# Optimization experiments

Measured on AMD Instinct MI355X. Metric: run time of the kernel, lower is better.

The kernel has to match this reference:

```python
import jax, jax.numpy as jnp
import numpy as np
from jax.scipy.special import logsumexp

B = 4096        # batch_size
D = 512         # feature dim
C = 128         # class_num
TEMP_F = 0.5
TEMP_L = 1.0
LAMBDA1 = 0.5
LAMBDA2 = 0.5
COS_EPS = 1e-8  # torch CosineSimilarity eps


def setup_inputs() -> dict:
    key = jax.random.key(0)
    k1, k2, k3, k4, k5 = jax.random.split(key, 5)
    return {
        "h1": jax.random.normal(k1, (B, D), dtype=jnp.float32),
        "h2": jax.random.normal(k2, (B, D), dtype=jnp.float32),
        "q1": jax.random.uniform(k3, (B, C), dtype=jnp.float32),
        "q2": jax.random.uniform(k4, (B, C), dtype=jnp.float32),
        "confidence": jax.random.uniform(k5, (B,), dtype=jnp.float32),
    }


def _ntxent_from_sim(sim, half):
    """NT-Xent per-row loss given full sim matrix [2*half, 2*half].

    Key identity: logits row r = [pos_r, negatives_r] where negatives exclude
    cols {r, partner(r)} and pos_r = sim[r, partner(r)]. Hence
    CE(logits, 0) = logsumexp over row excluding only the diagonal, minus pos.
    """
    N = 2 * half
    pos = jnp.concatenate([jnp.diagonal(sim, offset=half),
                           jnp.diagonal(sim, offset=-half)], axis=0)  # [N]
    eye = jnp.eye(N, dtype=bool)
    sim_masked = jnp.where(eye, -jnp.inf, sim)
    lse = logsumexp(sim_masked, axis=1)  # [N]
    return lse - pos  # per-row CE loss


def _forward_feature(h_i, h_j, confidence):
    b = h_i.shape[0]
    h = jnp.concatenate([h_i, h_j], axis=0)              # [2B, D]
    sim = jnp.matmul(h, h.T) / TEMP_F                     # [2B, 2B]
    loss = _ntxent_from_sim(sim, b)                       # [2B]
    loss = loss * jnp.tile(confidence, 2)                 # confidence.repeat(2)
    return loss.mean()


def _forward_label(q_i, q_j):
    c = q_i.shape[1]
    p_i = q_i.sum(0)
    p_i = p_i / p_i.sum()
    ne_i = jnp.log(jnp.float32(c)) + (p_i * jnp.log(p_i)).sum()
    p_j = q_j.sum(0)
    p_j = p_j / p_j.sum()
    ne_j = jnp.log(jnp.float32(c)) + (p_j * jnp.log(p_j)).sum()
    entropy = ne_i + ne_j

    q = jnp.concatenate([q_i.T, q_j.T], axis=0)           # [2C, B]
    norms = jnp.linalg.norm(q, axis=1)                    # [2C]
    denom = jnp.maximum(norms[:, None] * norms[None, :], COS_EPS)
    sim = (q @ q.T) / denom / TEMP_L                      # [2C, 2C]
    loss = _ntxent_from_sim(sim, c)                       # [2C]
    return loss.mean() + entropy


def reference(h1, h2, q1, q2, confidence):
    loss_feat = _forward_feature(h1, h2, confidence)
    loss_label = _forward_label(q1, q2)
    return LAMBDA1 * loss_feat + LAMBDA2 * loss_label
```

## Files before the change

### kernel.cpp

```cpp
#include <hip/hip_runtime.h>

typedef __attribute__((ext_vector_type(8))) short short8;
typedef __attribute__((ext_vector_type(4))) float f32x4;

#define NROW 8192
#define D_SZ 512

#define HB_OFF     0u
#define SPARTL_OFF 0u
#define SGRAM_OFF  2097152u
#define PSUMP_OFF  2359296u
#define FPART_OFF  2363392u
#define POS_OFF    8388608u
#define MPART_OFF  8421376u
#define SPARTF_OFF 8683520u

__device__ __forceinline__ unsigned short f32_to_bf16(float f) {
  unsigned int u = __float_as_uint(f);
  u = (u + 0x7FFFu + ((u >> 16) & 1u)) >> 16;
  return (unsigned short)u;
}

__global__ void convert_kernel(const float* __restrict__ h1, const float* __restrict__ h2,
                               unsigned short* __restrict__ hb) {
  int tid = blockIdx.x * 256 + threadIdx.x;
  float4 v = (tid < 524288) ? reinterpret_cast<const float4*>(h1)[tid]
                            : reinterpret_cast<const float4*>(h2)[tid - 524288];
  ushort4 o;
  o.x = f32_to_bf16(v.x); o.y = f32_to_bf16(v.y);
  o.z = f32_to_bf16(v.z); o.w = f32_to_bf16(v.w);
  reinterpret_cast<ushort4*>(hb)[tid] = o;
}

__global__ __launch_bounds__(256, 2) void feature_kernel(
    const short* __restrict__ hb, float* __restrict__ pos,
    float* __restrict__ mpart, float* __restrict__ spart) {
  __shared__ short lds_s[32 * 512];
  const int tid = threadIdx.x;
  const int w = tid >> 6;
  const int lane = tid & 63;
  const int lo16 = lane & 15;
  const int grp = lane >> 4;
  const int cz = blockIdx.x;
  const int bt = blockIdx.y;
  const int Rw = bt * 128 + w * 32;

  short8 A[2][16];
#pragma unroll
  for (int rt = 0; rt < 2; ++rt) {
    const short* ab = hb + (Rw + rt * 16 + lo16) * D_SZ + grp * 8;
#pragma unroll
    for (int kk = 0; kk < 16; ++kk)
      A[rt][kk] = *reinterpret_cast<const short8*>(ab + kk * 32);
  }
#pragma unroll
  for (int rt = 0; rt < 2; ++rt)
#pragma unroll
    for (int kk = 0; kk < 16; ++kk)
      asm volatile("" : "+v"(A[rt][kk]));

  float m0 = -INFINITY, m1 = -INFINITY, s0 = 0.f, s1 = 0.f;
  const int r0 = Rw + lo16;
  const int r1 = Rw + 16 + lo16;
  const int p0 = (r0 + 4096) & 8191;
  const int p1 = (r1 + 4096) & 8191;
  const int swz = (lo16 & 7) << 3;

#pragma unroll 1
  for (int g = 0; g < 32; ++g) {
    const int cg = cz * 1024 + g * 32;
    __syncthreads();
#pragma unroll
    for (int i = 0; i < 8; ++i) {
      int ch = i * 256 + tid;
      int col = ch >> 6, k8 = ch & 63;
      short8 v = *reinterpret_cast<const short8*>(hb + (cg + col) * D_SZ + k8 * 8);
      int dst = col * D_SZ + ((k8 * 8) ^ ((col & 7) << 3));
      *reinterpret_cast<short8*>(&lds_s[dst]) = v;
    }
    __syncthreads();

    f32x4 acc00 = {0,0,0,0}, acc01 = {0,0,0,0}, acc10 = {0,0,0,0}, acc11 = {0,0,0,0};
#pragma unroll
    for (int kk = 0; kk < 16; ++kk) {
      const int k = kk * 32 + grp * 8;
      short8 B0 = *reinterpret_cast<const short8*>(&lds_s[lo16 * D_SZ + (k ^ swz)]);
      short8 B1 = *reinterpret_cast<const short8*>(&lds_s[(16 + lo16) * D_SZ + (k ^ swz)]);
      acc00 = __builtin_amdgcn_mfma_f32_16x16x32_bf16(B0, A[0][kk], acc00, 0, 0, 0);
      acc01 = __builtin_amdgcn_mfma_f32_16x16x32_bf16(B0, A[1][kk], acc01, 0, 0, 0);
      acc10 = __builtin_amdgcn_mfma_f32_16x16x32_bf16(B1, A[0][kk], acc10, 0, 0, 0);
      acc11 = __builtin_amdgcn_mfma_f32_16x16x32_bf16(B1, A[1][kk], acc11, 0, 0, 0);
    }

    const int cbase = cg + grp * 4;
    {
      float v[8];
#pragma unroll
      for (int j = 0; j < 4; ++j) { v[j] = acc00[j] * 2.f; v[4 + j] = acc10[j] * 2.f; }
#pragma unroll
      for (int j = 0; j < 4; ++j) {
        int c0 = cbase + j, c1 = cbase + 16 + j;
        if (c0 == p0) pos[r0] = v[j];
        if (c1 == p0) pos[r0] = v[4 + j];
        if (c0 == r0) v[j] = -INFINITY;
        if (c1 == r0) v[4 + j] = -INFINITY;
      }
      float tm = v[0];
#pragma unroll
      for (int i = 1; i < 8; ++i) tm = fmaxf(tm, v[i]);
      tm = fmaxf(tm, __shfl_xor(tm, 16));
      tm = fmaxf(tm, __shfl_xor(tm, 32));
      float mn = fmaxf(m0, tm);
      float e = 0.f;
#pragma unroll
      for (int i = 0; i < 8; ++i) e += __expf(v[i] - mn);
      e += __shfl_xor(e, 16);
      e += __shfl_xor(e, 32);
      s0 = s0 * __expf(m0 - mn) + e;
      m0 = mn;
    }
    {
      float v[8];
#pragma unroll
      for (int j = 0; j < 4; ++j) { v[j] = acc01[j] * 2.f; v[4 + j] = acc11[j] * 2.f; }
#pragma unroll
      for (int j = 0; j < 4; ++j) {
        int c0 = cbase + j, c1 = cbase + 16 + j;
        if (c0 == p1) pos[r1] = v[j];
        if (c1 == p1) pos[r1] = v[4 + j];
        if (c0 == r1) v[j] = -INFINITY;
        if (c1 == r1) v[4 + j] = -INFINITY;
      }
      float tm = v[0];
#pragma unroll
      for (int i = 1; i < 8; ++i) tm = fmaxf(tm, v[i]);
      tm = fmaxf(tm, __shfl_xor(tm, 16));
      tm = fmaxf(tm, __shfl_xor(tm, 32));
      float mn = fmaxf(m1, tm);
      float e = 0.f;
#pragma unroll
      for (int i = 0; i < 8; ++i) e += __expf(v[i] - mn);
      e += __shfl_xor(e, 16);
      e += __shfl_xor(e, 32);
      s1 = s1 * __expf(m1 - mn) + e;
      m1 = mn;
    }
  }

  if (grp == 0) {
    mpart[cz * NROW + r0] = m0; spart[cz * NROW + r0] = s0;
    mpart[cz * NROW + r1] = m1; spart[cz * NROW + r1] = s1;
  }
}

__global__ void combine_feature_kernel(const float* __restrict__ mpart,
                                       const float* __restrict__ spart,
                                       const float* __restrict__ pos,
                                       const float* __restrict__ conf,
                                       float* __restrict__ fpart) {
  __shared__ float red[256];
  int r = blockIdx.x * 256 + threadIdx.x;
  float M = -INFINITY;
#pragma unroll
  for (int k = 0; k < 8; ++k) M = fmaxf(M, mpart[k * NROW + r]);
  float S = 0.f;
#pragma unroll
  for (int k = 0; k < 8; ++k) S += spart[k * NROW + r] * __expf(mpart[k * NROW + r] - M);
  float lse = logf(S) + M;
  float loss = (lse - pos[r]) * conf[r & 4095];
  red[threadIdx.x] = loss;
  __syncthreads();
  for (int s = 128; s > 0; s >>= 1) {
    if (threadIdx.x < s) red[threadIdx.x] += red[threadIdx.x + s];
    __syncthreads();
  }
  if (threadIdx.x == 0) fpart[blockIdx.x] = red[0];
}

__global__ __launch_bounds__(256) void label_gemm_kernel(const float* __restrict__ q1,
                                                         const float* __restrict__ q2,
                                                         float* __restrict__ Spart) {
  __shared__ float As[32 * 64];
  __shared__ float Bs[32 * 32];
  const int t = threadIdx.x;
  const int kz = blockIdx.x >> 5;
  const int bi = (blockIdx.x & 31) >> 3;
  const int bj = blockIdx.x & 7;
  const int tx = t & 15, ty = t >> 4;
  float a[4][2];
#pragma unroll
  for (int dr = 0; dr < 4; ++dr)
#pragma unroll
    for (int dc = 0; dc < 2; ++dc) a[dr][dc] = 0.f;

  for (int ch = 0; ch < 16; ++ch) {
    const int kbase = kz * 512 + ch * 32;
    __syncthreads();
#pragma unroll
    for (int i = 0; i < 8; ++i) {
      int e = i * 256 + t;
      int kr = e >> 6, j = e & 63;
      int ca = bi * 64 + j;
      As[kr * 64 + j] = (ca < 128) ? q1[(kbase + kr) * 128 + ca]
                                   : q2[(kbase + kr) * 128 + ca - 128];
    }
#pragma unroll
    for (int i = 0; i < 4; ++i) {
      int e = i * 256 + t;
      int kr = e >> 5, j = e & 31;
      int cb = bj * 32 + j;
      Bs[kr * 32 + j] = (cb < 128) ? q1[(kbase + kr) * 128 + cb]
                                   : q2[(kbase + kr) * 128 + cb - 128];
    }
    __syncthreads();
#pragma unroll 8
    for (int k = 0; k < 32; ++k) {
      float4 Av = *reinterpret_cast<const float4*>(&As[k * 64 + ty * 4]);
      float2 Bv = *reinterpret_cast<const float2*>(&Bs[k * 32 + tx * 2]);
      a[0][0] += Av.x * Bv.x; a[0][1] += Av.x * Bv.y;
      a[1][0] += Av.y * Bv.x; a[1][1] += Av.y * Bv.y;
      a[2][0] += Av.z * Bv.x; a[2][1] += Av.z * Bv.y;
      a[3][0] += Av.w * Bv.x; a[3][1] += Av.w * Bv.y;
    }
  }
  float* outp = Spart + kz * 65536;
#pragma unroll
  for (int dr = 0; dr < 4; ++dr) {
    int r = bi * 64 + ty * 4 + dr;
    int c = bj * 32 + tx * 2;
    outp[r * 256 + c] = a[dr][0];
    outp[r * 256 + c + 1] = a[dr][1];
  }
}

__global__ void label_prep_kernel(const float* __restrict__ q1, const float* __restrict__ q2,
                                  const float* __restrict__ Spart, float* __restrict__ S,
                                  float* __restrict__ psum_part) {
  const int b = blockIdx.x, t = threadIdx.x;
  if (b < 256) {
    int e = b * 256 + t;
    float acc = 0.f;
#pragma unroll
    for (int kz = 0; kz < 8; ++kz) acc += Spart[kz * 65536 + e];
    S[e] = acc;
  } else {
    __shared__ float sd[256];
    int idx = b - 256;
    const float* q = (idx < 4) ? q1 : q2;
    int col = t & 127, half = t >> 7;
    int rbase = (idx & 3) * 1024 + half * 512;
    float acc = 0.f;
    for (int i = 0; i < 512; ++i) acc += q[(rbase + i) * 128 + col];
    sd[t] = acc;
    __syncthreads();
    if (t < 128) psum_part[idx * 128 + col] = sd[t] + sd[t + 128];
  }
}

__global__ __launch_bounds__(256) void label_final_kernel(
    const float* __restrict__ S, const float* __restrict__ psum_part,
    const float* __restrict__ fpart, float* __restrict__ out) {
  __shared__ float nrm[256], red[256], redl[256];
  __shared__ float entropy_sh, feat_sh;
  const int t = threadIdx.x;
  nrm[t] = sqrtf(fmaxf(S[t * 257], 0.f));
  const float* pp = psum_part + (t >> 7) * 512 + (t & 127);
  float v = pp[0] + pp[128] + pp[256] + pp[384];
  red[t] = v;
  redl[t] = v * logf(fmaxf(v, 1e-30f));
  __syncthreads();
  for (int s = 64; s > 0; s >>= 1) {
    if ((t & 127) < s) { red[t] += red[t + s]; redl[t] += redl[t + s]; }
    __syncthreads();
  }
  if (t == 0) {
    float tot1 = red[0], tot2 = red[128];
    float ne1 = logf(128.f) + (redl[0] / tot1 - logf(tot1));
    float ne2 = logf(128.f) + (redl[128] / tot2 - logf(tot2));
    entropy_sh = ne1 + ne2;
  }
  __syncthreads();
  red[t] = (t < 32) ? fpart[t] : 0.f;
  __syncthreads();
  for (int s = 128; s > 0; s >>= 1) {
    if (t < s) red[t] += red[t + s];
    __syncthreads();
  }
  if (t == 0) feat_sh = red[0];
  __syncthreads();

  const float nr = nrm[t];
  const float* Srow = S + t * 256;
  const int partner = (t + 128) & 255;
  float m = -INFINITY;
  for (int c = 0; c < 256; ++c) {
    if (c == t) continue;
    float sv = Srow[c] / fmaxf(nr * nrm[c], 1e-8f);
    m = fmaxf(m, sv);
  }
  float ssum = 0.f, posv = 0.f;
  for (int c = 0; c < 256; ++c) {
    float sv = Srow[c] / fmaxf(nr * nrm[c], 1e-8f);
    if (c == partner) posv = sv;
    if (c != t) ssum += __expf(sv - m);
  }
  float loss_r = (logf(ssum) + m) - posv;
  __syncthreads();
  red[t] = loss_r;
  __syncthreads();
  for (int s = 128; s > 0; s >>= 1) {
    if (t < s) red[t] += red[t + s];
    __syncthreads();
  }
  if (t == 0)
    out[0] = 0.5f * (feat_sh / 8192.f) + 0.5f * (red[0] / 256.f + entropy_sh);
}

extern "C" void kernel_launch(void* const* d_in, const int* in_sizes, int n_in,
                              void* d_out, int out_size, void* d_ws, size_t ws_size,
                              hipStream_t stream) {
  const float* h1 = (const float*)d_in[0];
  const float* h2 = (const float*)d_in[1];
  const float* q1 = (const float*)d_in[2];
  const float* q2 = (const float*)d_in[3];
  const float* conf = (const float*)d_in[4];
  float* out = (float*)d_out;
  char* ws = (char*)d_ws;

  unsigned short* hb = (unsigned short*)(ws + HB_OFF);
  float* pos    = (float*)(ws + POS_OFF);
  float* mpart  = (float*)(ws + MPART_OFF);
  float* spartf = (float*)(ws + SPARTF_OFF);
  float* SpartL = (float*)(ws + SPARTL_OFF);
  float* Sgram  = (float*)(ws + SGRAM_OFF);
  float* psump  = (float*)(ws + PSUMP_OFF);
  float* fpart  = (float*)(ws + FPART_OFF);

  convert_kernel<<<4096, 256, 0, stream>>>(h1, h2, hb);
  feature_kernel<<<dim3(8, 64), 256, 0, stream>>>((const short*)hb, pos, mpart, spartf);
  combine_feature_kernel<<<32, 256, 0, stream>>>(mpart, spartf, pos, conf, fpart);
  label_gemm_kernel<<<256, 256, 0, stream>>>(q1, q2, SpartL);
  label_prep_kernel<<<264, 256, 0, stream>>>(q1, q2, SpartL, Sgram, psump);
  label_final_kernel<<<1, 256, 0, stream>>>(Sgram, psump, fpart, out);
}
```

Measured before the change: 272.9 us.

## Retile feature GEMM into 256x256 LDS-staged blocks with async double buffering

The feature kernel is rewritten to use 512-thread blocks computing 256x256 output tiles. Both operands are staged through double-buffered LDS using global_load_lds, and the online logsumexp update runs once per 256-column tile instead of once per 32-column step. The label GEMM is retiled to 64x64 output tiles with a 16-way K split, and the prep and final kernels are adjusted to match. This is meant to raise MFMA reuse and overlap loads with compute, at the cost of a large register footprint (128 accumulator floats per thread) and more partial buffers.

```diff
diff --git a/kernel.cpp b/kernel.cpp
--- a/kernel.cpp
+++ b/kernel.cpp
@@ -8,12 +8,17 @@
 
 #define HB_OFF     0u
 #define SPARTL_OFF 0u
-#define SGRAM_OFF  2097152u
-#define PSUMP_OFF  2359296u
-#define FPART_OFF  2363392u
+#define SGRAM_OFF  4194304u
+#define PSUMP_OFF  4456448u
+#define FPART_OFF  4472832u
 #define POS_OFF    8388608u
 #define MPART_OFF  8421376u
 #define SPARTF_OFF 8683520u
+
+#define GLOAD_LDS(gp, lp)                                     \
+  __builtin_amdgcn_global_load_lds(                           \
+      (const __attribute__((address_space(1))) void*)(gp),    \
+      (__attribute__((address_space(3))) void*)(lp), 16, 0, 0)
 
 __device__ __forceinline__ unsigned short f32_to_bf16(float f) {
   unsigned int u = __float_as_uint(f);
@@ -32,125 +37,160 @@
   reinterpret_cast<ushort4*>(hb)[tid] = o;
 }
 
-__global__ __launch_bounds__(256, 2) void feature_kernel(
+__global__ __launch_bounds__(512, 2) void feature_kernel(
     const short* __restrict__ hb, float* __restrict__ pos,
     float* __restrict__ mpart, float* __restrict__ spart) {
-  __shared__ short lds_s[32 * 512];
+  __shared__ short lds_s[2][2][16384];
   const int tid = threadIdx.x;
   const int w = tid >> 6;
   const int lane = tid & 63;
   const int lo16 = lane & 15;
   const int grp = lane >> 4;
+  const int lo7 = lo16 & 7;
+  const int wr = w >> 2;
+  const int wc = w & 3;
   const int cz = blockIdx.x;
   const int bt = blockIdx.y;
-  const int Rw = bt * 128 + w * 32;
-
-  short8 A[2][16];
-#pragma unroll
-  for (int rt = 0; rt < 2; ++rt) {
-    const short* ab = hb + (Rw + rt * 16 + lo16) * D_SZ + grp * 8;
-#pragma unroll
-    for (int kk = 0; kk < 16; ++kk)
-      A[rt][kk] = *reinterpret_cast<const short8*>(ab + kk * 32);
-  }
-#pragma unroll
-  for (int rt = 0; rt < 2; ++rt)
-#pragma unroll
-    for (int kk = 0; kk < 16; ++kk)
-      asm volatile("" : "+v"(A[rt][kk]));
-
-  float m0 = -INFINITY, m1 = -INFINITY, s0 = 0.f, s1 = 0.f;
-  const int r0 = Rw + lo16;
-  const int r1 = Rw + 16 + lo16;
-  const int p0 = (r0 + 4096) & 8191;
-  const int p1 = (r1 + 4096) & 8191;
-  const int swz = (lo16 & 7) << 3;
+  const int R0 = bt * 256;
+  const int CZ0 = cz * 1024;
+
+  const int srow = tid >> 3;
+  const int csrc = (tid & 7) ^ (srow & 7);
+  const short* baseA = hb + (size_t)(R0 + srow) * D_SZ + csrc * 8;
+  const short* baseB = hb + (size_t)(CZ0 + srow) * D_SZ + csrc * 8;
+
+#define STAGE_STEP(ct_, bk_, buf_) do {                        \
+    const short* sa_ = baseA + (bk_) * 64;                     \
+    const short* sb_ = baseB + (ct_) * 131072 + (bk_) * 64;    \
+    short* da_ = &lds_s[buf_][0][tid * 8];                     \
+    short* db_ = &lds_s[buf_][1][tid * 8];                     \
+    GLOAD_LDS(sa_, da_);                  GLOAD_LDS(sb_, db_);                  \
+    GLOAD_LDS(sa_ + 32768, da_ + 4096);   GLOAD_LDS(sb_ + 32768, db_ + 4096);   \
+    GLOAD_LDS(sa_ + 65536, da_ + 8192);   GLOAD_LDS(sb_ + 65536, db_ + 8192);   \
+    GLOAD_LDS(sa_ + 98304, da_ + 12288);  GLOAD_LDS(sb_ + 98304, db_ + 12288);  \
+  } while (0)
+
+  float mrun[8], srun[8];
+#pragma unroll
+  for (int rf = 0; rf < 8; ++rf) { mrun[rf] = -INFINITY; srun[rf] = 0.f; }
+
+  f32x4 acc[4][8];
+#pragma unroll
+  for (int cf = 0; cf < 4; ++cf)
+#pragma unroll
+    for (int rf = 0; rf < 8; ++rf) acc[cf][rf] = (f32x4){0, 0, 0, 0};
+
+  const int rowbaseA = (wr * 128 + lo16) * 64;
+  const int colbaseB = (wc * 64 + lo16) * 64;
+
+  STAGE_STEP(0, 0, 0);
+  __syncthreads();
 
 #pragma unroll 1
-  for (int g = 0; g < 32; ++g) {
-    const int cg = cz * 1024 + g * 32;
-    __syncthreads();
-#pragma unroll
-    for (int i = 0; i < 8; ++i) {
-      int ch = i * 256 + tid;
-      int col = ch >> 6, k8 = ch & 63;
-      short8 v = *reinterpret_cast<const short8*>(hb + (cg + col) * D_SZ + k8 * 8);
-      int dst = col * D_SZ + ((k8 * 8) ^ ((col & 7) << 3));
-      *reinterpret_cast<short8*>(&lds_s[dst]) = v;
-    }
-    __syncthreads();
-
-    f32x4 acc00 = {0,0,0,0}, acc01 = {0,0,0,0}, acc10 = {0,0,0,0}, acc11 = {0,0,0,0};
-#pragma unroll
-    for (int kk = 0; kk < 16; ++kk) {
-      const int k = kk * 32 + grp * 8;
-      short8 B0 = *reinterpret_cast<const short8*>(&lds_s[lo16 * D_SZ + (k ^ swz)]);
-      short8 B1 = *reinterpret_cast<const short8*>(&lds_s[(16 + lo16) * D_SZ + (k ^ swz)]);
-      acc00 = __builtin_amdgcn_mfma_f32_16x16x32_bf16(B0, A[0][kk], acc00, 0, 0, 0);
-      acc01 = __builtin_amdgcn_mfma_f32_16x16x32_bf16(B0, A[1][kk], acc01, 0, 0, 0);
-      acc10 = __builtin_amdgcn_mfma_f32_16x16x32_bf16(B1, A[0][kk], acc10, 0, 0, 0);
-      acc11 = __builtin_amdgcn_mfma_f32_16x16x32_bf16(B1, A[1][kk], acc11, 0, 0, 0);
-    }
-
-    const int cbase = cg + grp * 4;
-    {
-      float v[8];
-#pragma unroll
-      for (int j = 0; j < 4; ++j) { v[j] = acc00[j] * 2.f; v[4 + j] = acc10[j] * 2.f; }
-#pragma unroll
-      for (int j = 0; j < 4; ++j) {
-        int c0 = cbase + j, c1 = cbase + 16 + j;
-        if (c0 == p0) pos[r0] = v[j];
-        if (c1 == p0) pos[r0] = v[4 + j];
-        if (c0 == r0) v[j] = -INFINITY;
-        if (c1 == r0) v[4 + j] = -INFINITY;
+  for (int step = 0; step < 32; ++step) {
+    const int ct = step >> 3, bk = step & 7, buf = step & 1;
+    if (step < 31) {
+      const int s2 = step + 1;
+      STAGE_STEP(s2 >> 3, s2 & 7, buf ^ 1);
+    }
+    const short* pA = &lds_s[buf][0][0];
+    const short* pB = &lds_s[buf][1][0];
+
+#pragma unroll
+    for (int ksub = 0; ksub < 2; ++ksub) {
+      const int chsw = ((ksub * 4 + grp) ^ lo7) * 8;
+      short8 cf_[4], rf_[8];
+#pragma unroll
+      for (int cf = 0; cf < 4; ++cf)
+        cf_[cf] = *reinterpret_cast<const short8*>(&pB[colbaseB + cf * 1024 + chsw]);
+#pragma unroll
+      for (int rf = 0; rf < 8; ++rf)
+        rf_[rf] = *reinterpret_cast<const short8*>(&pA[rowbaseA + rf * 1024 + chsw]);
+#pragma unroll
+      for (int cf = 0; cf < 4; ++cf)
+#pragma unroll
+        for (int rf = 0; rf < 8; ++rf)
+          acc[cf][rf] = __builtin_amdgcn_mfma_f32_16x16x32_bf16(cf_[cf], rf_[rf],
+                                                                acc[cf][rf], 0, 0, 0);
+    }
+
+    if (bk == 7) {
+      const int C0 = CZ0 + ct * 256;
+      const bool hd = (C0 == R0);
+      const bool hp = (C0 == ((R0 + 4096) & 8191));
+#pragma unroll
+      for (int rf = 0; rf < 8; ++rf) {
+        const int row = R0 + wr * 128 + rf * 16 + lo16;
+        float v[16];
+#pragma unroll
+        for (int cf = 0; cf < 4; ++cf)
+#pragma unroll
+          for (int j = 0; j < 4; ++j) v[cf * 4 + j] = acc[cf][rf][j] * 2.f;
+        if (hd || hp) {
+          const int prow = (row + 4096) & 8191;
+#pragma unroll
+          for (int cf = 0; cf < 4; ++cf)
+#pragma unroll
+            for (int j = 0; j < 4; ++j) {
+              const int c = C0 + wc * 64 + cf * 16 + grp * 4 + j;
+              if (hp && c == prow) pos[row] = v[cf * 4 + j];
+              if (hd && c == row) v[cf * 4 + j] = -INFINITY;
+            }
+        }
+        float tm = v[0];
+#pragma unroll
+        for (int i = 1; i < 16; ++i) tm = fmaxf(tm, v[i]);
+        const float mn = fmaxf(mrun[rf], tm);
+        float e = 0.f;
+#pragma unroll
+        for (int i = 0; i < 16; ++i) e += __expf(v[i] - mn);
+        srun[rf] = srun[rf] * __expf(mrun[rf] - mn) + e;
+        mrun[rf] = mn;
+#pragma unroll
+        for (int cf = 0; cf < 4; ++cf) acc[cf][rf] = (f32x4){0, 0, 0, 0};
       }
-      float tm = v[0];
-#pragma unroll
-      for (int i = 1; i < 8; ++i) tm = fmaxf(tm, v[i]);
-      tm = fmaxf(tm, __shfl_xor(tm, 16));
-      tm = fmaxf(tm, __shfl_xor(tm, 32));
-      float mn = fmaxf(m0, tm);
-      float e = 0.f;
-#pragma unroll
-      for (int i = 0; i < 8; ++i) e += __expf(v[i] - mn);
-      e += __shfl_xor(e, 16);
-      e += __shfl_xor(e, 32);
-      s0 = s0 * __expf(m0 - mn) + e;
-      m0 = mn;
-    }
-    {
-      float v[8];
-#pragma unroll
-      for (int j = 0; j < 4; ++j) { v[j] = acc01[j] * 2.f; v[4 + j] = acc11[j] * 2.f; }
-#pragma unroll
-      for (int j = 0; j < 4; ++j) {
-        int c0 = cbase + j, c1 = cbase + 16 + j;
-        if (c0 == p1) pos[r1] = v[j];
-        if (c1 == p1) pos[r1] = v[4 + j];
-        if (c0 == r1) v[j] = -INFINITY;
-        if (c1 == r1) v[4 + j] = -INFINITY;
-      }
-      float tm = v[0];
-#pragma unroll
-      for (int i = 1; i < 8; ++i) tm = fmaxf(tm, v[i]);
-      tm = fmaxf(tm, __shfl_xor(tm, 16));
-      tm = fmaxf(tm, __shfl_xor(tm, 32));
-      float mn = fmaxf(m1, tm);
-      float e = 0.f;
-#pragma unroll
-      for (int i = 0; i < 8; ++i) e += __expf(v[i] - mn);
-      e += __shfl_xor(e, 16);
-      e += __shfl_xor(e, 32);
-      s1 = s1 * __expf(m1 - mn) + e;
-      m1 = mn;
-    }
-  }
-
+    }
+    __syncthreads();
+  }
+
+#pragma unroll
+  for (int rf = 0; rf < 8; ++rf) {
+#pragma unroll
+    for (int off = 16; off <= 32; off <<= 1) {
+      float mo = __shfl_xor(mrun[rf], off), so = __shfl_xor(srun[rf], off);
+      float mn = fmaxf(mrun[rf], mo);
+      srun[rf] = srun[rf] * __expf(mrun[rf] - mn) + so * __expf(mo - mn);
+      mrun[rf] = mn;
+    }
+  }
+
+  float* marr = reinterpret_cast<float*>(&lds_s[0][0][0]);
+  float* sarr = marr + 1024;
   if (grp == 0) {
-    mpart[cz * NROW + r0] = m0; spart[cz * NROW + r0] = s0;
-    mpart[cz * NROW + r1] = m1; spart[cz * NROW + r1] = s1;
-  }
+#pragma unroll
+    for (int rf = 0; rf < 8; ++rf) {
+      const int idx = ((wr * 4 + wc) * 8 + rf) * 16 + lo16;
+      marr[idx] = mrun[rf];
+      sarr[idx] = srun[rf];
+    }
+  }
+  __syncthreads();
+  if (tid < 256) {
+    const int row = tid;
+    const int wr2 = row >> 7, rf2 = (row >> 4) & 7, lo2 = row & 15;
+    float M = -INFINITY, S = 0.f;
+#pragma unroll
+    for (int wc2 = 0; wc2 < 4; ++wc2) {
+      const int idx = ((wr2 * 4 + wc2) * 8 + rf2) * 16 + lo2;
+      const float m = marr[idx], s = sarr[idx];
+      const float mn = fmaxf(M, m);
+      S = S * __expf(M - mn) + s * __expf(m - mn);
+      M = mn;
+    }
+    mpart[cz * NROW + R0 + row] = M;
+    spart[cz * NROW + R0 + row] = S;
+  }
+#undef STAGE_STEP
 }
 
 __global__ void combine_feature_kernel(const float* __restrict__ mpart,
@@ -181,55 +221,50 @@
                                                          const float* __restrict__ q2,
                                                          float* __restrict__ Spart) {
   __shared__ float As[32 * 64];
-  __shared__ float Bs[32 * 32];
+  __shared__ float Bs[32 * 64];
   const int t = threadIdx.x;
-  const int kz = blockIdx.x >> 5;
-  const int bi = (blockIdx.x & 31) >> 3;
-  const int bj = blockIdx.x & 7;
+  const int kz = blockIdx.x >> 4;
+  const int bi = (blockIdx.x >> 2) & 3;
+  const int bj = blockIdx.x & 3;
   const int tx = t & 15, ty = t >> 4;
-  float a[4][2];
+  float a[4][4];
 #pragma unroll
   for (int dr = 0; dr < 4; ++dr)
 #pragma unroll
-    for (int dc = 0; dc < 2; ++dc) a[dr][dc] = 0.f;
-
-  for (int ch = 0; ch < 16; ++ch) {
-    const int kbase = kz * 512 + ch * 32;
+    for (int dc = 0; dc < 4; ++dc) a[dr][dc] = 0.f;
+
+  for (int ch = 0; ch < 8; ++ch) {
+    const int kbase = kz * 256 + ch * 32;
     __syncthreads();
 #pragma unroll
     for (int i = 0; i < 8; ++i) {
       int e = i * 256 + t;
       int kr = e >> 6, j = e & 63;
       int ca = bi * 64 + j;
+      int cb = bj * 64 + j;
       As[kr * 64 + j] = (ca < 128) ? q1[(kbase + kr) * 128 + ca]
                                    : q2[(kbase + kr) * 128 + ca - 128];
-    }
-#pragma unroll
-    for (int i = 0; i < 4; ++i) {
-      int e = i * 256 + t;
-      int kr = e >> 5, j = e & 31;
-      int cb = bj * 32 + j;
-      Bs[kr * 32 + j] = (cb < 128) ? q1[(kbase + kr) * 128 + cb]
+      Bs[kr * 64 + j] = (cb < 128) ? q1[(kbase + kr) * 128 + cb]
                                    : q2[(kbase + kr) * 128 + cb - 128];
     }
     __syncthreads();
 #pragma unroll 8
     for (int k = 0; k < 32; ++k) {
       float4 Av = *reinterpret_cast<const float4*>(&As[k * 64 + ty * 4]);
-      float2 Bv = *reinterpret_cast<const float2*>(&Bs[k * 32 + tx * 2]);
-      a[0][0] += Av.x * Bv.x; a[0][1] += Av.x * Bv.y;
-      a[1][0] += Av.y * Bv.x; a[1][1] += Av.y * Bv.y;
-      a[2][0] += Av.z * Bv.x; a[2][1] += Av.z * Bv.y;
-      a[3][0] += Av.w * Bv.x; a[3][1] += Av.w * Bv.y;
-    }
-  }
-  float* outp = Spart + kz * 65536;
+      float4 Bv = *reinterpret_cast<const float4*>(&Bs[k * 64 + tx * 4]);
+      a[0][0] += Av.x * Bv.x; a[0][1] += Av.x * Bv.y; a[0][2] += Av.x * Bv.z; a[0][3] += Av.x * Bv.w;
+      a[1][0] += Av.y * Bv.x; a[1][1] += Av.y * Bv.y; a[1][2] += Av.y * Bv.z; a[1][3] += Av.y * Bv.w;
+      a[2][0] += Av.z * Bv.x; a[2][1] += Av.z * Bv.y; a[2][2] += Av.z * Bv.z; a[2][3] += Av.z * Bv.w;
+      a[3][0] += Av.w * Bv.x; a[3][1] += Av.w * Bv.y; a[3][2] += Av.w * Bv.z; a[3][3] += Av.w * Bv.w;
+    }
+  }
+  float* outp = Spart + (size_t)kz * 65536;
 #pragma unroll
   for (int dr = 0; dr < 4; ++dr) {
     int r = bi * 64 + ty * 4 + dr;
-    int c = bj * 32 + tx * 2;
-    outp[r * 256 + c] = a[dr][0];
-    outp[r * 256 + c + 1] = a[dr][1];
+    int c = bj * 64 + tx * 4;
+    float4 o = {a[dr][0], a[dr][1], a[dr][2], a[dr][3]};
+    *reinterpret_cast<float4*>(&outp[r * 256 + c]) = o;
   }
 }
 
@@ -241,16 +276,16 @@
     int e = b * 256 + t;
     float acc = 0.f;
 #pragma unroll
-    for (int kz = 0; kz < 8; ++kz) acc += Spart[kz * 65536 + e];
+    for (int kz = 0; kz < 16; ++kz) acc += Spart[(size_t)kz * 65536 + e];
     S[e] = acc;
   } else {
     __shared__ float sd[256];
     int idx = b - 256;
-    const float* q = (idx < 4) ? q1 : q2;
-    int col = t & 127, half = t >> 7;
-    int rbase = (idx & 3) * 1024 + half * 512;
+    const float* q = (idx < 16) ? q1 : q2;
+    int col = t & 127, rh = t >> 7;
+    int rbase = (idx & 15) * 256 + rh;
     float acc = 0.f;
-    for (int i = 0; i < 512; ++i) acc += q[(rbase + i) * 128 + col];
+    for (int i = 0; i < 128; ++i) acc += q[(rbase + 2 * i) * 128 + col];
     sd[t] = acc;
     __syncthreads();
     if (t < 128) psum_part[idx * 128 + col] = sd[t] + sd[t + 128];
@@ -264,8 +299,10 @@
   __shared__ float entropy_sh, feat_sh;
   const int t = threadIdx.x;
   nrm[t] = sqrtf(fmaxf(S[t * 257], 0.f));
-  const float* pp = psum_part + (t >> 7) * 512 + (t & 127);
-  float v = pp[0] + pp[128] + pp[256] + pp[384];
+  const float* pp = psum_part + (t >> 7) * 2048 + (t & 127);
+  float v = 0.f;
+#pragma unroll
+  for (int i = 0; i < 16; ++i) v += pp[i * 128];
   red[t] = v;
   redl[t] = v * logf(fmaxf(v, 1e-30f));
   __syncthreads();
@@ -337,9 +374,9 @@
   float* fpart  = (float*)(ws + FPART_OFF);
 
   convert_kernel<<<4096, 256, 0, stream>>>(h1, h2, hb);
-  feature_kernel<<<dim3(8, 64), 256, 0, stream>>>((const short*)hb, pos, mpart, spartf);
+  feature_kernel<<<dim3(8, 32), 512, 0, stream>>>((const short*)hb, pos, mpart, spartf);
   combine_feature_kernel<<<32, 256, 0, stream>>>(mpart, spartf, pos, conf, fpart);
   label_gemm_kernel<<<256, 256, 0, stream>>>(q1, q2, SpartL);
-  label_prep_kernel<<<264, 256, 0, stream>>>(q1, q2, SpartL, Sgram, psump);
+  label_prep_kernel<<<288, 256, 0, stream>>>(q1, q2, SpartL, Sgram, psump);
   label_final_kernel<<<1, 256, 0, stream>>>(Sgram, psump, fpart, out);
 }
```

Result: faster. 220.6 us (-19.2%).
